# Kernel tuning notes

Hardware: AMD Instinct MI355X
Metric: run time of the kernel (lower is better)

Reference implementation:

```python
import jax, jax.numpy as jnp
import numpy as np

A = 200000   # atoms
B = 400000   # directed bonds
H = 300      # hidden_size
AF = 133     # atom_fdim
BF = 147     # bond_fdim
DEPTH = 4    # message passing depth -> DEPTH-1 W_h layers
M = 4096     # molecules in batch


def setup_inputs() -> dict:
    key = jax.random.key(0)
    ks = jax.random.split(key, 10)
    s = 0.05
    f_atoms = jax.random.normal(ks[0], (A, AF), jnp.float32)
    f_bonds = jax.random.normal(ks[1], (B, BF), jnp.float32)
    b_src = jax.random.randint(ks[2], (B,), 0, A, jnp.int32)
    b_dst = jax.random.randint(ks[3], (B,), 0, A, jnp.int32)
    # reverse-bond pairing: bond 2i <-> 2i+1
    b2revb = (jnp.arange(B, dtype=jnp.int32) ^ 1)
    mol_ids = jnp.sort(jax.random.randint(ks[4], (A,), 0, M, jnp.int32))
    W_i_atom = jax.random.normal(ks[5], (AF, H), jnp.float32) * s
    W_i_bond = jax.random.normal(ks[6], (BF, H), jnp.float32) * s
    W_h = jax.random.normal(ks[7], (DEPTH - 1, H, H), jnp.float32) * s
    W_o = jax.random.normal(ks[8], (3 * H, H), jnp.float32) * s
    b_o = jnp.zeros((H,), jnp.float32)
    return dict(f_atoms=f_atoms, f_bonds=f_bonds, W_i_atom=W_i_atom,
                W_i_bond=W_i_bond, W_h=W_h, W_o=W_o, b_o=b_o,
                b_src=b_src, b_dst=b_dst, b2revb=b2revb, mol_ids=mol_ids)


def reference(f_atoms, f_bonds, W_i_atom, W_i_bond, W_h, W_o, b_o,
              b_src, b_dst, b2revb, mol_ids):
    relu = jax.nn.relu
    input_atom = relu(f_atoms @ W_i_atom)   # [A, H]
    input_bond = relu(f_bonds @ W_i_bond)   # [B, H]

    def step(message, Wd):
        # scatter-sum incoming bond messages onto destination atoms
        a_msg = jax.ops.segment_sum(message, b_dst, num_segments=A)  # [A, H]
        # gather back to bonds, subtract reverse-bond message (D-MPNN)
        m = a_msg[b_src] - message[b2revb]                           # [B, H]
        return relu(input_bond + m @ Wd), None

    message, _ = jax.lax.scan(step, input_bond, W_h)  # DEPTH-1 iterations

    a_msg = jax.ops.segment_sum(message, b_dst, num_segments=A)      # [A, H]
    a_input = jnp.concatenate([input_atom, a_msg, input_atom * a_msg], axis=-1)
    atom_h = relu(a_input @ W_o + b_o)                               # [A, H]

    # mean readout per molecule
    sums = jax.ops.segment_sum(atom_h, mol_ids, num_segments=M)      # [M, H]
    counts = jax.ops.segment_sum(jnp.ones((A,), atom_h.dtype), mol_ids, num_segments=M)
    return sums / jnp.clip(counts, 1.0)[:, None]
```

## Files before the change

### kernel.cpp

```cpp
#include <hip/hip_runtime.h>
#include <stdint.h>

#define H   300
#define HP  320
#define CAP 32

using bf8 = __attribute__((ext_vector_type(8))) short;
using s4  = __attribute__((ext_vector_type(4))) short;
using f4  = __attribute__((ext_vector_type(4))) float;

__device__ __forceinline__ float bf2f(unsigned short u){
    union { unsigned int i; float f; } v; v.i = ((unsigned int)u) << 16; return v.f;
}
__device__ __forceinline__ unsigned short f2bf(float x){
    unsigned int u = __builtin_bit_cast(unsigned int, x);
    u = (u + 0x7FFFu + ((u >> 16) & 1u)) >> 16;
    return (unsigned short)u;
}

__global__ void fill_k(const int* __restrict__ b_dst, int* __restrict__ cnt,
                       int* __restrict__ bucket, int nB){
    int e = blockIdx.x * 256 + threadIdx.x;
    if (e >= nB) return;
    int d = b_dst[e];
    int slot = atomicAdd(&cnt[d], 1);
    if (slot < CAP) bucket[(long)d * CAP + slot] = e;
}

__global__ void prep_wt(const float* __restrict__ W, unsigned short* __restrict__ Wt,
                        int Kact, int Kp){
    int idx = blockIdx.x * 256 + threadIdx.x;
    if (idx >= 320 * Kp) return;
    int t  = idx / (320 * 32);
    int r  = idx % (320 * 32);
    int n  = r / 32, kk = r % 32;
    int k  = t * 32 + kk;
    float v = (n < H && k < Kact) ? W[(long)k * H + n] : 0.f;
    Wt[idx] = f2bf(v);
}

__global__ void prep_wto(const float* __restrict__ W, unsigned short* __restrict__ Wt){
    int idx = blockIdx.x * 256 + threadIdx.x;
    if (idx >= 320 * 960) return;
    int t  = idx / (320 * 32);
    int r  = idx % (320 * 32);
    int n  = r / 32, kk = r % 32;
    int k  = t * 32 + kk;
    int sec = k / HP, ksec = k % HP;
    float v = (n < H && ksec < H) ? W[((long)sec * H + ksec) * H + n] : 0.f;
    Wt[idx] = f2bf(v);
}

__global__ __launch_bounds__(256)
void conv_in(const float* __restrict__ X, int rows, int Kact,
             unsigned short* __restrict__ Y){
    int t = blockIdx.x * 256 + threadIdx.x;
    if (t >= rows * 20) return;
    int row = t / 20, c = t % 20;
    int k0 = c * 8;
    bf8 v;
    #pragma unroll
    for (int j = 0; j < 8; j++){
        int k = k0 + j;
        float f = (k < Kact) ? X[(long)row * Kact + k] : 0.f;
        v[j] = (short)f2bf(f);
    }
    *(bf8*)(Y + (long)row * 160 + k0) = v;
}

template<int RL, int BM, int EPI>
__global__ __launch_bounds__(256, 1)
void bstat_k(const unsigned short* __restrict__ A,
             const unsigned short* __restrict__ Wt,
             unsigned short* __restrict__ outb,
             int nTiles)
{
    constexpr int T     = RL / 32;
    constexpr int MF    = BM / 32;
    constexpr int TILEB = BM * RL * 2;

    __shared__ char ldsB[T * 10240];
    __shared__ char ldsA[2][TILEB];

    const int tid  = threadIdx.x;
    const int w    = tid >> 6;
    const int wm   = w >> 1, wn = w & 1;
    const int lane = tid & 63;
    const int lr   = lane & 15;
    const int g    = lane >> 4;
    const int nh   = blockIdx.x & 1;

    for (int idx = tid; idx < T * 640; idx += 256){
        int t  = idx / 640;
        int r  = idx - t * 640;
        int gg = r / 160;
        int n  = r - gg * 160;
        bf8 v = *(const bf8*)(Wt + ((long)t * 320 + nh * 160 + n) * 32 + gg * 8);
        *(bf8*)(ldsB + (long)idx * 16) = v;
    }

    auto dma = [&](int t, int buf){
        const char* g0 = (const char*)A + (long)t * TILEB + tid * 16;
        char* l0 = ldsA[buf] + (w * 64) * 16;
        #pragma unroll
        for (int rd = 0; rd < 5; rd++)
            __builtin_amdgcn_global_load_lds(
                (const __attribute__((address_space(1))) void*)(g0 + rd * 4096),
                (__attribute__((address_space(3))) void*)(l0 + rd * 4096),
                16, 0, 0);
    };

    int tile = blockIdx.x >> 1;
    if (tile < nTiles) dma(tile, 0);
    __syncthreads();

    int buf = 0;
    for (; tile < nTiles; tile += 128){
        int nt = tile + 128;
        if (nt < nTiles) dma(nt, buf ^ 1);

        f4 acc[MF][5];
        #pragma unroll
        for (int mf = 0; mf < MF; mf++)
            #pragma unroll
            for (int nf = 0; nf < 5; nf++)
                acc[mf][nf] = (f4){0.f, 0.f, 0.f, 0.f};

        #pragma unroll
        for (int t = 0; t < T; t++){
            bf8 bfr[5], af[MF];
            const char* bb = ldsB + (((t * 4 + g) * 160) + wn * 80 + lr) * 16;
            #pragma unroll
            for (int nf = 0; nf < 5; nf++)
                bfr[nf] = *(const bf8*)(bb + nf * 256);
            #pragma unroll
            for (int mf = 0; mf < MF; mf++){
                int row = wm * (BM / 2) + mf * 16 + lr;
                af[mf] = *(const bf8*)(ldsA[buf] + row * (RL * 2) + (t * 4 + g) * 16);
            }
            #pragma unroll
            for (int mf = 0; mf < MF; mf++)
                #pragma unroll
                for (int nf = 0; nf < 5; nf++)
                    acc[mf][nf] = __builtin_amdgcn_mfma_f32_16x16x32_bf16(
                        bfr[nf], af[mf], acc[mf][nf], 0, 0, 0);
        }

        #pragma unroll
        for (int mf = 0; mf < MF; mf++){
            const long row = (long)tile * BM + wm * (BM / 2) + mf * 16 + lr;
            #pragma unroll
            for (int nf = 0; nf < 5; nf++){
                const int colg = nh * 160 + wn * 80 + nf * 16 + g * 4;
                s4 v4;
                #pragma unroll
                for (int q = 0; q < 4; q++){
                    float v = acc[mf][nf][q];
                    if constexpr (EPI == 0) v = fmaxf(v, 0.f);
                    v4[q] = (short)f2bf(v);
                }
                *(s4*)(outb + row * HP + colg) = v4;
            }
        }
        __syncthreads();
        buf ^= 1;
    }
}

__global__ __launch_bounds__(256, 4)
void gemm_wo(const unsigned short* __restrict__ A0,
             const unsigned short* __restrict__ A1,
             const unsigned short* __restrict__ Wt,
             const float* __restrict__ b_o,
             unsigned short* __restrict__ outb,
             int nTiles)
{
    __shared__ char lds0[32 * 640];
    __shared__ char lds1[32 * 640];

    const int tid  = threadIdx.x;
    const int w    = tid >> 6;
    const int lane = tid & 63;
    const int lr   = lane & 15;
    const int g    = lane >> 4;

    int tile = blockIdx.x;
    if (tile >= nTiles) return;
    const long rowBase = (long)tile * 32;

    auto stageA = [&](const unsigned short* src, char* dst){
        const char* gb = (const char*)(src + rowBase * HP);
        bf8 st[5];
        #pragma unroll
        for (int i = 0; i < 5; i++)
            st[i] = *(const bf8*)(gb + (i * 256 + tid) * 16);
        #pragma unroll
        for (int i = 0; i < 5; i++){
            int f = i * 256 + tid;
            int row = f / 40, c = f % 40;
            *(bf8*)(dst + row * 640 + ((c ^ (row & 7)) << 4)) = st[i];
        }
    };

    bf8 bb[2][5];
    auto loadB = [&](int t, bf8 (&dst)[5]){
        const unsigned short* base = Wt + ((long)t * 320) * 32 + g * 8;
        #pragma unroll
        for (int n = 0; n < 5; n++)
            dst[n] = *(const bf8*)(base + (w * 80 + n * 16 + lr) * 32);
    };

    stageA(A0, lds0);
    stageA(A1, lds1);
    loadB(0, bb[0]);
    __syncthreads();

    f4 acc[2][5];
    #pragma unroll
    for (int m = 0; m < 2; m++)
        #pragma unroll
        for (int n = 0; n < 5; n++)
            acc[m][n] = (f4){0.f, 0.f, 0.f, 0.f};

    #pragma unroll
    for (int sec = 0; sec < 3; ++sec){
        if (sec > 0){
            __syncthreads();
            loadB(sec * 10, bb[0]);
        }
        loadB(sec * 10 + 1, bb[1]);

        #pragma unroll
        for (int i = 0; i < 10; i++){
            bf8 af[2];
            #pragma unroll
            for (int m = 0; m < 2; m++){
                const int row = m * 16 + lr;
                const int off = row * 640 + (((i * 4 + g) ^ (row & 7)) << 4);
                if (sec == 0){
                    af[m] = *(const bf8*)(lds0 + off);
                } else if (sec == 1){
                    af[m] = *(const bf8*)(lds1 + off);
                } else {
                    bf8 a = *(const bf8*)(lds0 + off);
                    bf8 b = *(const bf8*)(lds1 + off);
                    #pragma unroll
                    for (int q = 0; q < 8; q++)
                        af[m][q] = (short)f2bf(bf2f((unsigned short)a[q]) *
                                               bf2f((unsigned short)b[q]));
                }
            }
            #pragma unroll
            for (int m = 0; m < 2; m++)
                #pragma unroll
                for (int n = 0; n < 5; n++)
                    acc[m][n] = __builtin_amdgcn_mfma_f32_16x16x32_bf16(
                        bb[i & 1][n], af[m], acc[m][n], 0, 0, 0);
            if (i + 2 < 10) loadB(sec * 10 + i + 2, bb[i & 1]);
        }
    }

    #pragma unroll
    for (int m = 0; m < 2; m++){
        const long row = rowBase + m * 16 + lr;
        #pragma unroll
        for (int n = 0; n < 5; n++){
            const int colg = w * 80 + n * 16 + g * 4;
            s4 v4;
            #pragma unroll
            for (int q = 0; q < 4; q++){
                int col = colg + q;
                float v = acc[m][n][q];
                v += (col < H ? b_o[col] : 0.f);
                v4[q] = (short)f2bf(fmaxf(v, 0.f));
            }
            *(s4*)(outb + row * HP + colg) = v4;
        }
    }
}

__global__ __launch_bounds__(256)
void comb_k(const unsigned short* __restrict__ MW,
            const unsigned short* __restrict__ bond_in,
            const int* __restrict__ b_src, const int* __restrict__ b2revb,
            const int* __restrict__ cnt, const int* __restrict__ bucket,
            unsigned short* __restrict__ out, int nB){
    int t = blockIdx.x * 256 + threadIdx.x;
    if (t >= nB * 40) return;
    int e = t / 40, ch = t % 40;
    int k0 = ch * 8;
    int s   = b_src[e];
    int rev = b2revb[e];
    int dg = cnt[s]; if (dg > CAP) dg = CAP;
    long base = (long)s * CAP;
    int be0 = 0, be1 = 0, be2 = 0, be3 = 0;
    if (dg > 0) be0 = bucket[base + 0];
    if (dg > 1) be1 = bucket[base + 1];
    if (dg > 2) be2 = bucket[base + 2];
    if (dg > 3) be3 = bucket[base + 3];
    bf8 bi = *(const bf8*)(bond_in + (long)e * HP + k0);
    bf8 rv = *(const bf8*)(MW + (long)rev * HP + k0);
    bf8 m0, m1, m2, m3;
    if (dg > 0) m0 = *(const bf8*)(MW + (long)be0 * HP + k0);
    if (dg > 1) m1 = *(const bf8*)(MW + (long)be1 * HP + k0);
    if (dg > 2) m2 = *(const bf8*)(MW + (long)be2 * HP + k0);
    if (dg > 3) m3 = *(const bf8*)(MW + (long)be3 * HP + k0);
    float sacc[8];
    #pragma unroll
    for (int q = 0; q < 8; q++)
        sacc[q] = bf2f((unsigned short)bi[q]) - bf2f((unsigned short)rv[q]);
    auto addv = [&](bf8 mm){
        #pragma unroll
        for (int q = 0; q < 8; q++) sacc[q] += bf2f((unsigned short)mm[q]);
    };
    if (dg > 0) addv(m0);
    if (dg > 1) addv(m1);
    if (dg > 2) addv(m2);
    if (dg > 3) addv(m3);
    for (int j = 4; j < dg; ++j){
        int be = bucket[base + j];
        addv(*(const bf8*)(MW + (long)be * HP + k0));
    }
    bf8 v;
    #pragma unroll
    for (int q = 0; q < 8; q++) v[q] = (short)f2bf(fmaxf(sacc[q], 0.f));
    *(bf8*)(out + (long)e * HP + k0) = v;
}

__global__ __launch_bounds__(256)
void amsg_k(const unsigned short* __restrict__ msg, const int* __restrict__ cnt,
            const int* __restrict__ bucket,
            unsigned short* __restrict__ amsg, int nA){
    int t = blockIdx.x * 256 + threadIdx.x;
    if (t >= nA * 40) return;
    int a = t / 40, ch = t % 40;
    int k0 = ch * 8;
    int dg = cnt[a]; if (dg > CAP) dg = CAP;
    long base = (long)a * CAP;
    int be0 = 0, be1 = 0, be2 = 0, be3 = 0;
    if (dg > 0) be0 = bucket[base + 0];
    if (dg > 1) be1 = bucket[base + 1];
    if (dg > 2) be2 = bucket[base + 2];
    if (dg > 3) be3 = bucket[base + 3];
    bf8 m0, m1, m2, m3;
    if (dg > 0) m0 = *(const bf8*)(msg + (long)be0 * HP + k0);
    if (dg > 1) m1 = *(const bf8*)(msg + (long)be1 * HP + k0);
    if (dg > 2) m2 = *(const bf8*)(msg + (long)be2 * HP + k0);
    if (dg > 3) m3 = *(const bf8*)(msg + (long)be3 * HP + k0);
    float s[8];
    #pragma unroll
    for (int q = 0; q < 8; q++) s[q] = 0.f;
    auto addv = [&](bf8 mm){
        #pragma unroll
        for (int q = 0; q < 8; q++) s[q] += bf2f((unsigned short)mm[q]);
    };
    if (dg > 0) addv(m0);
    if (dg > 1) addv(m1);
    if (dg > 2) addv(m2);
    if (dg > 3) addv(m3);
    for (int j = 4; j < dg; ++j)
        addv(*(const bf8*)(msg + (long)bucket[base + j] * HP + k0));
    bf8 va;
    #pragma unroll
    for (int q = 0; q < 8; q++) va[q] = (short)f2bf(s[q]);
    *(bf8*)(amsg + (long)a * HP + k0) = va;
}

__global__ __launch_bounds__(320)
void readout_k(const unsigned short* __restrict__ atom_h,
               const int* __restrict__ mol_ids, int nAtoms,
               float* __restrict__ out){
    int m = blockIdx.x;
    int t = threadIdx.x;
    int lo = 0, hi = nAtoms;
    while (lo < hi){ int mid = (lo + hi) >> 1; if (mol_ids[mid] < m) lo = mid + 1; else hi = mid; }
    int lo2 = lo, hi2 = nAtoms;
    while (lo2 < hi2){ int mid = (lo2 + hi2) >> 1; if (mol_ids[mid] < m + 1) lo2 = mid + 1; else hi2 = mid; }
    if (t < H){
        float s = 0.f;
        for (int a = lo; a < lo2; ++a) s += bf2f(atom_h[(long)a * HP + t]);
        int c2 = lo2 - lo;
        out[(long)m * H + t] = s / (float)(c2 > 0 ? c2 : 1);
    }
}

extern "C" void kernel_launch(void* const* d_in, const int* in_sizes, int n_in,
                              void* d_out, int out_size, void* d_ws, size_t ws_size,
                              hipStream_t stream){
    const float* f_atoms  = (const float*)d_in[0];
    const float* f_bonds  = (const float*)d_in[1];
    const float* W_i_atom = (const float*)d_in[2];
    const float* W_i_bond = (const float*)d_in[3];
    const float* W_h      = (const float*)d_in[4];
    const float* W_o      = (const float*)d_in[5];
    const float* b_o      = (const float*)d_in[6];
    const int* b_src   = (const int*)d_in[7];
    const int* b_dst   = (const int*)d_in[8];
    const int* b2revb  = (const int*)d_in[9];
    const int* mol_ids = (const int*)d_in[10];

    const int nA = in_sizes[10];
    const int nB = in_sizes[7];
    const int nM = out_size / H;

    char* p = (char*)d_ws;
    auto alloc = [&](size_t bytes){ char* q = p; p += (bytes + 255) & ~(size_t)255; return q; };
    unsigned short* Wt_ia = (unsigned short*)alloc((size_t)320 * 160 * 2);
    unsigned short* Wt_ib = (unsigned short*)alloc((size_t)320 * 160 * 2);
    unsigned short* Wt_h  = (unsigned short*)alloc((size_t)3 * 320 * 320 * 2);
    unsigned short* Wt_o  = (unsigned short*)alloc((size_t)320 * 960 * 2);
    int* cnt    = (int*)alloc((size_t)nA * 4);
    int* bucket = (int*)alloc((size_t)nA * CAP * 4);
    unsigned short* input_atom = (unsigned short*)alloc((size_t)nA * HP * 2);
    unsigned short* input_bond = (unsigned short*)alloc((size_t)nB * HP * 2);
    unsigned short* msgA = (unsigned short*)alloc((size_t)nB * HP * 2);
    unsigned short* MW   = (unsigned short*)alloc((size_t)nB * HP * 2);
    unsigned short* fa_bf  = MW;
    unsigned short* fb_bf  = MW + (size_t)nA * 160;
    unsigned short* amsg   = MW;
    unsigned short* atom_h = input_bond;

    if ((size_t)(p - (char*)d_ws) > ws_size) return;

    hipMemsetAsync(cnt, 0, (size_t)nA * 4, stream);
    fill_k<<<dim3((nB + 255) / 256), dim3(256), 0, stream>>>(b_dst, cnt, bucket, nB);

    prep_wt<<<dim3((320*160 + 255)/256), dim3(256), 0, stream>>>(W_i_atom, Wt_ia, 133, 160);
    prep_wt<<<dim3((320*160 + 255)/256), dim3(256), 0, stream>>>(W_i_bond, Wt_ib, 147, 160);
    for (int d = 0; d < 3; d++)
        prep_wt<<<dim3((320*320 + 255)/256), dim3(256), 0, stream>>>(
            W_h + (size_t)d * H * H, Wt_h + (size_t)d * 320 * 320, 300, 320);
    prep_wto<<<dim3((320*960 + 255)/256), dim3(256), 0, stream>>>(W_o, Wt_o);
    conv_in<<<dim3((nA*20 + 255)/256), dim3(256), 0, stream>>>(f_atoms, nA, 133, fa_bf);
    conv_in<<<dim3((nB*20 + 255)/256), dim3(256), 0, stream>>>(f_bonds, nB, 147, fb_bf);

    bstat_k<160,64,0><<<dim3(256), dim3(256), 0, stream>>>(
        fa_bf, Wt_ia, input_atom, nA / 64);
    bstat_k<160,64,0><<<dim3(256), dim3(256), 0, stream>>>(
        fb_bf, Wt_ib, input_bond, nB / 64);

    const int combGrid = (nB * 40 + 255) / 256;
    const unsigned short* msg_cur = input_bond;
    for (int d = 0; d < 3; d++){
        bstat_k<320,32,1><<<dim3(256), dim3(256), 0, stream>>>(
            msg_cur, Wt_h + (size_t)d * 320 * 320, MW, nB / 32);
        comb_k<<<dim3(combGrid), dim3(256), 0, stream>>>(
            MW, input_bond, b_src, b2revb, cnt, bucket, msgA, nB);
        msg_cur = msgA;
    }

    amsg_k<<<dim3((nA * 40 + 255) / 256), dim3(256), 0, stream>>>(
        msgA, cnt, bucket, amsg, nA);

    gemm_wo<<<dim3(nA / 32), dim3(256), 0, stream>>>(
        input_atom, amsg, Wt_o, b_o, atom_h, nA / 32);

    readout_k<<<dim3(nM), dim3(320), 0, stream>>>(atom_h, mol_ids, nA, (float*)d_out);
}
```

Before: 2.135 ms.

## Make gemm_wo persistent with double-buffered direct global-to-LDS loads of pre-swizzled inputs

The W_o GEMM becomes a persistent kernel on 512 blocks that loops over tiles and double-buffers its A operands in LDS, using global_load_lds DMA to prefetch the next tile while computing the current one. To let the DMA copy rows straight into the swizzled LDS layout, the producers of input_atom and amsg now write their outputs with 16-byte chunks XOR-swizzled by row. This is meant to remove the register-staged LDS writes and hide load latency behind the MFMA work. The cost is a doubled LDS footprint with lower occupancy (launch bounds drop from 4 to 2 blocks), and it relies on no other consumer reading those buffers in plain layout.

```diff
diff --git a/kernel.cpp b/kernel.cpp
--- a/kernel.cpp
+++ b/kernel.cpp
@@ -156,10 +156,16 @@
                 #pragma unroll
                 for (int q = 0; q < 4; q++){
                     float v = acc[mf][nf][q];
-                    if constexpr (EPI == 0) v = fmaxf(v, 0.f);
+                    if constexpr (EPI != 1) v = fmaxf(v, 0.f);
                     v4[q] = (short)f2bf(v);
                 }
-                *(s4*)(outb + row * HP + colg) = v4;
+                if constexpr (EPI == 2){
+                    int ch = colg >> 3;
+                    *(s4*)(outb + row * HP + ((long)(ch ^ ((int)row & 7)) << 3)
+                           + (colg & 7)) = v4;
+                } else {
+                    *(s4*)(outb + row * HP + colg) = v4;
+                }
             }
         }
         __syncthreads();
@@ -167,7 +173,7 @@
     }
 }
 
-__global__ __launch_bounds__(256, 4)
+__global__ __launch_bounds__(256, 2)
 void gemm_wo(const unsigned short* __restrict__ A0,
              const unsigned short* __restrict__ A1,
              const unsigned short* __restrict__ Wt,
@@ -175,8 +181,7 @@
              unsigned short* __restrict__ outb,
              int nTiles)
 {
-    __shared__ char lds0[32 * 640];
-    __shared__ char lds1[32 * 640];
+    __shared__ char lds[2][2][20480];
 
     const int tid  = threadIdx.x;
     const int w    = tid >> 6;
@@ -184,21 +189,21 @@
     const int lr   = lane & 15;
     const int g    = lane >> 4;
 
-    int tile = blockIdx.x;
-    if (tile >= nTiles) return;
-    const long rowBase = (long)tile * 32;
-
-    auto stageA = [&](const unsigned short* src, char* dst){
-        const char* gb = (const char*)(src + rowBase * HP);
-        bf8 st[5];
-        #pragma unroll
-        for (int i = 0; i < 5; i++)
-            st[i] = *(const bf8*)(gb + (i * 256 + tid) * 16);
-        #pragma unroll
-        for (int i = 0; i < 5; i++){
-            int f = i * 256 + tid;
-            int row = f / 40, c = f % 40;
-            *(bf8*)(dst + row * 640 + ((c ^ (row & 7)) << 4)) = st[i];
+    auto dma = [&](int t, int buf){
+        const char* g0 = (const char*)(A0 + (long)t * 32 * HP) + tid * 16;
+        const char* g1 = (const char*)(A1 + (long)t * 32 * HP) + tid * 16;
+        char* l0 = lds[buf][0] + (w * 64) * 16;
+        char* l1 = lds[buf][1] + (w * 64) * 16;
+        #pragma unroll
+        for (int rd = 0; rd < 5; rd++){
+            __builtin_amdgcn_global_load_lds(
+                (const __attribute__((address_space(1))) void*)(g0 + rd * 4096),
+                (__attribute__((address_space(3))) void*)(l0 + rd * 4096),
+                16, 0, 0);
+            __builtin_amdgcn_global_load_lds(
+                (const __attribute__((address_space(1))) void*)(g1 + rd * 4096),
+                (__attribute__((address_space(3))) void*)(l1 + rd * 4096),
+                16, 0, 0);
         }
     };
 
@@ -210,72 +215,79 @@
             dst[n] = *(const bf8*)(base + (w * 80 + n * 16 + lr) * 32);
     };
 
-    stageA(A0, lds0);
-    stageA(A1, lds1);
-    loadB(0, bb[0]);
+    int tile = blockIdx.x;
+    if (tile >= nTiles) return;
+    dma(tile, 0);
     __syncthreads();
 
-    f4 acc[2][5];
-    #pragma unroll
-    for (int m = 0; m < 2; m++)
-        #pragma unroll
-        for (int n = 0; n < 5; n++)
-            acc[m][n] = (f4){0.f, 0.f, 0.f, 0.f};
-
-    #pragma unroll
-    for (int sec = 0; sec < 3; ++sec){
-        if (sec > 0){
-            __syncthreads();
-            loadB(sec * 10, bb[0]);
+    int buf = 0;
+    for (; tile < nTiles; tile += (int)gridDim.x){
+        int nt = tile + (int)gridDim.x;
+        const bool hn = (nt < nTiles);
+        if (hn) dma(nt, buf ^ 1);
+
+        f4 acc[2][5];
+        #pragma unroll
+        for (int m = 0; m < 2; m++)
+            #pragma unroll
+            for (int n = 0; n < 5; n++)
+                acc[m][n] = (f4){0.f, 0.f, 0.f, 0.f};
+
+        #pragma unroll
+        for (int sec = 0; sec < 3; ++sec){
+            if (sec > 0) __syncthreads();
+            loadB(sec * 10 + 0, bb[0]);
+            loadB(sec * 10 + 1, bb[1]);
+
+            #pragma unroll
+            for (int i = 0; i < 10; i++){
+                bf8 af[2];
+                #pragma unroll
+                for (int m = 0; m < 2; m++){
+                    const int row = m * 16 + lr;
+                    const int off = row * 640 + (((i * 4 + g) ^ (row & 7)) << 4);
+                    if (sec == 0){
+                        af[m] = *(const bf8*)(lds[buf][0] + off);
+                    } else if (sec == 1){
+                        af[m] = *(const bf8*)(lds[buf][1] + off);
+                    } else {
+                        bf8 a = *(const bf8*)(lds[buf][0] + off);
+                        bf8 b = *(const bf8*)(lds[buf][1] + off);
+                        #pragma unroll
+                        for (int q = 0; q < 8; q++)
+                            af[m][q] = (short)f2bf(bf2f((unsigned short)a[q]) *
+                                                   bf2f((unsigned short)b[q]));
+                    }
+                }
+                #pragma unroll
+                for (int m = 0; m < 2; m++)
+                    #pragma unroll
+                    for (int n = 0; n < 5; n++)
+                        acc[m][n] = __builtin_amdgcn_mfma_f32_16x16x32_bf16(
+                            bb[i & 1][n], af[m], acc[m][n], 0, 0, 0);
+                if (i + 2 < 10) loadB(sec * 10 + i + 2, bb[i & 1]);
+            }
         }
-        loadB(sec * 10 + 1, bb[1]);
-
-        #pragma unroll
-        for (int i = 0; i < 10; i++){
-            bf8 af[2];
-            #pragma unroll
-            for (int m = 0; m < 2; m++){
-                const int row = m * 16 + lr;
-                const int off = row * 640 + (((i * 4 + g) ^ (row & 7)) << 4);
-                if (sec == 0){
-                    af[m] = *(const bf8*)(lds0 + off);
-                } else if (sec == 1){
-                    af[m] = *(const bf8*)(lds1 + off);
-                } else {
-                    bf8 a = *(const bf8*)(lds0 + off);
-                    bf8 b = *(const bf8*)(lds1 + off);
-                    #pragma unroll
-                    for (int q = 0; q < 8; q++)
-                        af[m][q] = (short)f2bf(bf2f((unsigned short)a[q]) *
-                                               bf2f((unsigned short)b[q]));
+
+        #pragma unroll
+        for (int m = 0; m < 2; m++){
+            const long row = (long)tile * 32 + m * 16 + lr;
+            #pragma unroll
+            for (int n = 0; n < 5; n++){
+                const int colg = w * 80 + n * 16 + g * 4;
+                s4 v4;
+                #pragma unroll
+                for (int q = 0; q < 4; q++){
+                    int col = colg + q;
+                    float v = acc[m][n][q];
+                    v += (col < H ? b_o[col] : 0.f);
+                    v4[q] = (short)f2bf(fmaxf(v, 0.f));
                 }
+                *(s4*)(outb + row * HP + colg) = v4;
             }
-            #pragma unroll
-            for (int m = 0; m < 2; m++)
-                #pragma unroll
-                for (int n = 0; n < 5; n++)
-                    acc[m][n] = __builtin_amdgcn_mfma_f32_16x16x32_bf16(
-                        bb[i & 1][n], af[m], acc[m][n], 0, 0, 0);
-            if (i + 2 < 10) loadB(sec * 10 + i + 2, bb[i & 1]);
         }
-    }
-
-    #pragma unroll
-    for (int m = 0; m < 2; m++){
-        const long row = rowBase + m * 16 + lr;
-        #pragma unroll
-        for (int n = 0; n < 5; n++){
-            const int colg = w * 80 + n * 16 + g * 4;
-            s4 v4;
-            #pragma unroll
-            for (int q = 0; q < 4; q++){
-                int col = colg + q;
-                float v = acc[m][n][q];
-                v += (col < H ? b_o[col] : 0.f);
-                v4[q] = (short)f2bf(fmaxf(v, 0.f));
-            }
-            *(s4*)(outb + row * HP + colg) = v4;
-        }
+        __syncthreads();
+        buf ^= 1;
     }
 }
 
@@ -363,7 +375,7 @@
     bf8 va;
     #pragma unroll
     for (int q = 0; q < 8; q++) va[q] = (short)f2bf(s[q]);
-    *(bf8*)(amsg + (long)a * HP + k0) = va;
+    *(bf8*)(amsg + (long)a * HP + ((long)(ch ^ (a & 7)) << 3)) = va;
 }
 
 __global__ __launch_bounds__(320)
@@ -434,7 +446,7 @@
     conv_in<<<dim3((nA*20 + 255)/256), dim3(256), 0, stream>>>(f_atoms, nA, 133, fa_bf);
     conv_in<<<dim3((nB*20 + 255)/256), dim3(256), 0, stream>>>(f_bonds, nB, 147, fb_bf);
 
-    bstat_k<160,64,0><<<dim3(256), dim3(256), 0, stream>>>(
+    bstat_k<160,64,2><<<dim3(256), dim3(256), 0, stream>>>(
         fa_bf, Wt_ia, input_atom, nA / 64);
     bstat_k<160,64,0><<<dim3(256), dim3(256), 0, stream>>>(
         fb_bf, Wt_ib, input_bond, nB / 64);
@@ -452,7 +464,7 @@
     amsg_k<<<dim3((nA * 40 + 255) / 256), dim3(256), 0, stream>>>(
         msgA, cnt, bucket, amsg, nA);
 
-    gemm_wo<<<dim3(nA / 32), dim3(256), 0, stream>>>(
+    gemm_wo<<<dim3(512), dim3(256), 0, stream>>>(
         input_atom, amsg, Wt_o, b_o, atom_h, nA / 32);
 
     readout_k<<<dim3(nM), dim3(320), 0, stream>>>(atom_h, mol_ids, nA, (float*)d_out);
```

Result: slower. 2.628 ms (+23.1%).
